# Kernel tuning notes

Measured on AMD Instinct MI355X. Metric: run time of the kernel, lower is better.

The kernel has to match this reference:

```python
import jax, jax.numpy as jnp
import numpy as np

NUM_EMBEDDINGS = 8192
EMBEDDING_DIM = 64
COMMITMENT_COST = 0.25


def setup_inputs() -> dict:
    key = jax.random.key(0)
    kx, ke = jax.random.split(key)
    x = jax.random.normal(kx, (32, 1024, EMBEDDING_DIM), dtype=jnp.float32)
    embeddings = jax.random.normal(ke, (NUM_EMBEDDINGS, EMBEDDING_DIM), dtype=jnp.float32)
    return {"x": x, "embeddings": embeddings}


def reference(x, embeddings):
    d = embeddings.shape[1]
    flat_x = x.reshape(-1, d)  # [N, D]
    # squared euclidean distances (argmin identical to cdist argmin):
    d2 = (
        jnp.sum(flat_x * flat_x, axis=-1, keepdims=True)
        - 2.0 * flat_x @ embeddings.T
        + jnp.sum(embeddings * embeddings, axis=-1)
    )
    encoding_indices = jnp.argmin(d2, axis=1)  # [N]
    quantized = embeddings[encoding_indices].reshape(x.shape)
    codebook_loss = jnp.mean((jax.lax.stop_gradient(quantized) - x) ** 2)
    commitment_loss = COMMITMENT_COST * jnp.mean((quantized - jax.lax.stop_gradient(x)) ** 2)
    loss = codebook_loss + commitment_loss
    # straight-through estimator
    quantized_st = x + jax.lax.stop_gradient(quantized - x)
    return quantized_st, loss, encoding_indices
```

## Files before the change

### kernel.cpp

```cpp
#include <hip/hip_runtime.h>
#include <hip/hip_bf16.h>
#include <float.h>

#define N_ROWS 32768
#define DIMS   64
#define K_EMB  8192
#define NT     (K_EMB / 16)
#define NQ     16
#define NTQ    (NT / NQ)
#define TSTAGE 4
#define NSTAGE (NTQ / TSTAGE)
#define RG     4
#define GAP_THR 1.5e-3f

typedef __attribute__((ext_vector_type(8))) short s8v;
typedef __attribute__((ext_vector_type(4))) float f4v;
typedef __attribute__((ext_vector_type(4))) int   i4v;

#define WS_EFRAG 0
#define WS_EN2   (2 * 1024 * 1024)
#define WS_IDX   (WS_EN2 + K_EMB * 4)
#define WS_KEY   (WS_IDX + N_ROWS * 4)
#define WS_BH    (WS_KEY + N_ROWS * 8)
#define WS_SH    (WS_BH + NQ * N_ROWS * 4)
#define WS_CH    (WS_SH + NQ * N_ROWS * 4)
#define WS_CTL   (WS_CH + NQ * N_ROWS * 4)
#define WS_WL    (WS_CTL + 16)

#define OUT_LOSS (N_ROWS * DIMS)
#define OUT_IDX  (N_ROWS * DIMS + 1)

__device__ inline short bfh(float v) {
    __hip_bfloat16 h = __float2bfloat16(v);
    return __builtin_bit_cast(short, h);
}
__device__ inline float bff(short s) {
    __hip_bfloat16 h = __builtin_bit_cast(__hip_bfloat16, s);
    return __bfloat162float(h);
}

__global__ void vq_prep(const float* __restrict__ emb, short* __restrict__ efrag,
                        float* __restrict__ en2, int4* __restrict__ ctl) {
    if (blockIdx.x == 0 && threadIdx.x == 0) *ctl = make_int4(0, 0, 0, 0);
    int gid = blockIdx.x * 256 + threadIdx.x;
    int t = gid >> 6, lane = gid & 63;
    int m = lane & 15, q = lane >> 4;
    const float* er = emb + (size_t)(t * 16 + m) * DIMS;
    s8v hi0, lo0, hi1, lo1;
    float ss = 0.f;
#pragma unroll
    for (int j = 0; j < 8; ++j) {
        float v0 = er[q * 8 + j];
        float v1 = er[32 + q * 8 + j];
        ss += v0 * v0 + v1 * v1;
        short h0 = bfh(v0); lo0[j] = bfh(v0 - bff(h0)); hi0[j] = h0;
        short h1 = bfh(v1); lo1[j] = bfh(v1 - bff(h1)); hi1[j] = h1;
    }
    s8v* base = (s8v*)efrag + (size_t)t * 4 * 64;
    base[0 * 64 + lane] = hi0;
    base[1 * 64 + lane] = hi1;
    base[2 * 64 + lane] = lo0;
    base[3 * 64 + lane] = lo1;
    ss += __shfl_xor(ss, 16, 64);
    ss += __shfl_xor(ss, 32, 64);
    if (q == 0) en2[t * 16 + m] = -0.5f * ss;
}

__global__ __launch_bounds__(256)
__attribute__((amdgpu_waves_per_eu(2, 3))) void vq_phase1(
    const float* __restrict__ x, const short* __restrict__ efrag,
    const float* __restrict__ en2,
    float* __restrict__ bh, float* __restrict__ sh, int* __restrict__ ch) {
    __shared__ __align__(16) char lds[2][TSTAGE * 4096];
    int tid = threadIdx.x, wid = tid >> 6, lane = tid & 63;
    int m = lane & 15, q = lane >> 4;
    int kh = blockIdx.y;
    int row0 = blockIdx.x * 256 + wid * 64;

    s8v ahi[RG][2], alo[RG][2];
#pragma unroll
    for (int g = 0; g < RG; ++g) {
        const float* xr = x + (size_t)(row0 + g * 16 + m) * DIMS + q * 8;
#pragma unroll
        for (int j = 0; j < 8; ++j) {
            float v0 = xr[j], v1 = xr[32 + j];
            short h0 = bfh(v0); alo[g][0][j] = bfh(v0 - bff(h0)); ahi[g][0][j] = h0;
            short h1 = bfh(v1); alo[g][1][j] = bfh(v1 - bff(h1)); ahi[g][1][j] = h1;
        }
    }

    float best[RG][4], sec[RG][4];
    int bc[RG][4];
#pragma unroll
    for (int g = 0; g < RG; ++g)
#pragma unroll
        for (int r = 0; r < 4; ++r) { best[g][r] = -FLT_MAX; sec[g][r] = -FLT_MAX; bc[g][r] = 0; }

    const char* gsrc = (const char*)efrag + (size_t)kh * NTQ * 4096;

#pragma unroll
    for (int i = 0; i < TSTAGE; ++i)
        __builtin_amdgcn_global_load_lds(
            (const __attribute__((address_space(1))) void*)(gsrc + i * 4096 + tid * 16),
            (__attribute__((address_space(3))) void*)(&lds[0][i * 4096 + tid * 16]),
            16, 0, 0);
    __syncthreads();

    for (int s = 0; s < NSTAGE; ++s) {
        int pb = s & 1;
        if (s + 1 < NSTAGE) {
            const char* gn = gsrc + (size_t)(s + 1) * TSTAGE * 4096;
#pragma unroll
            for (int i = 0; i < TSTAGE; ++i)
                __builtin_amdgcn_global_load_lds(
                    (const __attribute__((address_space(1))) void*)(gn + i * 4096 + tid * 16),
                    (__attribute__((address_space(3))) void*)(&lds[pb ^ 1][i * 4096 + tid * 16]),
                    16, 0, 0);
        }
        const i4v* B = (const i4v*)(lds[pb]);
        int tg0 = kh * NTQ + s * TSTAGE;
        const float* ep = en2 + (size_t)tg0 * 16 + m;
#pragma unroll
        for (int tt = 0; tt < TSTAGE; ++tt) {
            i4v b0 = B[tt * 256 + 0 * 64 + lane];
            i4v b1 = B[tt * 256 + 1 * 64 + lane];
            i4v b2 = B[tt * 256 + 2 * 64 + lane];
            i4v b3 = B[tt * 256 + 3 * 64 + lane];
            float c0 = ep[tt * 16];
            int cidx = (tg0 + tt) * 16 + m;
            f4v cinit = {c0, c0, c0, c0};
#pragma unroll
            for (int g = 0; g < RG; ++g) {
                f4v acc;
                acc = __builtin_amdgcn_mfma_f32_16x16x32_bf16(ahi[g][0], __builtin_bit_cast(s8v, b0), cinit, 0, 0, 0);
                acc = __builtin_amdgcn_mfma_f32_16x16x32_bf16(ahi[g][1], __builtin_bit_cast(s8v, b1), acc, 0, 0, 0);
                acc = __builtin_amdgcn_mfma_f32_16x16x32_bf16(ahi[g][0], __builtin_bit_cast(s8v, b2), acc, 0, 0, 0);
                acc = __builtin_amdgcn_mfma_f32_16x16x32_bf16(ahi[g][1], __builtin_bit_cast(s8v, b3), acc, 0, 0, 0);
                acc = __builtin_amdgcn_mfma_f32_16x16x32_bf16(alo[g][0], __builtin_bit_cast(s8v, b0), acc, 0, 0, 0);
                acc = __builtin_amdgcn_mfma_f32_16x16x32_bf16(alo[g][1], __builtin_bit_cast(s8v, b1), acc, 0, 0, 0);
#pragma unroll
                for (int r = 0; r < 4; ++r) {
                    float v = acc[r];
                    bool gt = v > best[g][r];
                    sec[g][r]  = __builtin_amdgcn_fmed3f(v, sec[g][r], best[g][r]);
                    best[g][r] = fmaxf(best[g][r], v);
                    bc[g][r]   = gt ? cidx : bc[g][r];
                }
            }
        }
        __syncthreads();
    }

#pragma unroll
    for (int g = 0; g < RG; ++g)
#pragma unroll
    for (int r = 0; r < 4; ++r) {
        float b = best[g][r], s = sec[g][r];
        int c = bc[g][r];
#pragma unroll
        for (int off = 1; off < 16; off <<= 1) {
            float ob = __shfl_xor(b, off, 64);
            float os = __shfl_xor(s, off, 64);
            int   oc = __shfl_xor(c, off, 64);
            float nb = fmaxf(b, ob);
            float ns = fmaxf(fminf(b, ob), fmaxf(s, os));
            bool take = (ob > b) || (ob == b && oc < c);
            c = take ? oc : c;
            b = nb; s = ns;
        }
        if (m == 0) {
            int o = kh * N_ROWS + row0 + g * 16 + q * 4 + r;
            bh[o] = b; sh[o] = s; ch[o] = c;
        }
    }
}

__global__ void vq_merge(const float* __restrict__ bh, const float* __restrict__ sh,
                         const int* __restrict__ ch, int* __restrict__ idx_buf,
                         unsigned long long* __restrict__ key8,
                         float* __restrict__ nbv,
                         int* __restrict__ wl, int* __restrict__ wl_count) {
    int row = blockIdx.x * 256 + threadIdx.x;
    float nb = bh[row];
    int   c  = ch[row];
    float ns = -FLT_MAX;
#pragma unroll
    for (int h = 1; h < NQ; ++h) {
        float b = bh[h * N_ROWS + row];
        int   cc = ch[h * N_ROWS + row];
        if (b > nb) { ns = nb; nb = b; c = cc; }
        else        { ns = fmaxf(ns, b); }
    }
#pragma unroll
    for (int h = 0; h < NQ; ++h) ns = fmaxf(ns, sh[h * N_ROWS + row]);
    idx_buf[row] = c;
    key8[row] = 0ULL;
    nbv[row] = nb;
    if (nb - ns < GAP_THR) {
        int pos = atomicAdd(wl_count, 1);
        wl[pos] = row;
    }
}

__global__ __launch_bounds__(64) void vq_fixup(
    const float* __restrict__ x, const float* __restrict__ emb,
    const float* __restrict__ en2, const float* __restrict__ nbv,
    unsigned long long* __restrict__ key8,
    const int* __restrict__ wl, const int* __restrict__ wl_count) {
    int lane = threadIdx.x;
    int cchunk = blockIdx.x & 127;
    int rslice = blockIdx.x >> 7;
    int cnt = *wl_count;
    if (rslice >= cnt) return;
    int c = cchunk * 64 + lane;
    const float4* er = (const float4*)(emb + (size_t)c * DIMS);
    float4 e[16];
#pragma unroll
    for (int qq = 0; qq < 16; ++qq) e[qq] = er[qq];
    float c0 = en2[c];
    for (int wi = rslice; wi < cnt; wi += 16) {
        int row = wl[wi];
        const float4* xr = (const float4*)(x + (size_t)row * DIMS);
        float d = 0.f;
#pragma unroll
        for (int qq = 0; qq < 16; ++qq) {
            float4 ee = e[qq];
            float4 xx = xr[qq];
            d += ee.x * xx.x + ee.y * xx.y + ee.z * xx.z + ee.w * xx.w;
        }
        float bf_ = d + c0;
        int bc_ = c;
#pragma unroll
        for (int off = 1; off < 64; off <<= 1) {
            float of = __shfl_xor(bf_, off, 64);
            int   oc = __shfl_xor(bc_, off, 64);
            if (of > bf_ || (of == bf_ && oc < bc_)) { bf_ = of; bc_ = oc; }
        }
        if (lane == 0 && bf_ >= nbv[row] - GAP_THR) {
            unsigned int u = __float_as_uint(bf_);
            unsigned int sb = ((int)u < 0) ? ~u : (u | 0x80000000u);
            unsigned long long key = ((unsigned long long)sb << 32) | (unsigned int)(~bc_);
            atomicMax(&key8[row], key);
        }
    }
}

__global__ void vq_gather(const float* __restrict__ x, const float* __restrict__ emb,
                          const int* __restrict__ idx_buf,
                          const unsigned long long* __restrict__ key8,
                          float* __restrict__ out, double* __restrict__ loss_acc,
                          int* __restrict__ done_count) {
    int row = blockIdx.x * blockDim.x + threadIdx.x;
    unsigned long long k = key8[row];
    int idx = k ? (int)(~(unsigned int)k) : idx_buf[row];
    const float4* ev = (const float4*)(emb + (size_t)idx * DIMS);
    const float4* xv = (const float4*)(x + (size_t)row * DIMS);
    float4* ov = (float4*)(out + (size_t)row * DIMS);
    float s = 0.f;
#pragma unroll
    for (int qq = 0; qq < 16; ++qq) {
        float4 ee = ev[qq];
        float4 xx = xv[qq];
        float dx = ee.x - xx.x, dy = ee.y - xx.y, dz = ee.z - xx.z, dw = ee.w - xx.w;
        s += dx * dx + dy * dy + dz * dz + dw * dw;
        ov[qq] = ee;
    }
#pragma unroll
    for (int off = 32; off > 0; off >>= 1) s += __shfl_down(s, off, 64);
    if ((threadIdx.x & 63) == 0) atomicAdd(loss_acc, (double)s);
    out[OUT_IDX + row] = (float)idx;
    __syncthreads();
    if (threadIdx.x == 0) {
        __threadfence();
        int d = atomicAdd(done_count, 1);
        if (d == (int)gridDim.x - 1) {
            double total = atomicAdd(loss_acc, 0.0);
            out[OUT_LOSS] = (float)(1.25 * total / (double)(N_ROWS * DIMS));
        }
    }
}

extern "C" void kernel_launch(void* const* d_in, const int* in_sizes, int n_in,
                              void* d_out, int out_size, void* d_ws, size_t ws_size,
                              hipStream_t stream) {
    const float* x   = (const float*)d_in[0];
    const float* emb = (const float*)d_in[1];
    float* out = (float*)d_out;
    char*  ws  = (char*)d_ws;

    short* efrag   = (short*)(ws + WS_EFRAG);
    float* en2     = (float*)(ws + WS_EN2);
    int*   idx_buf = (int*)(ws + WS_IDX);
    unsigned long long* key8 = (unsigned long long*)(ws + WS_KEY);
    float* bhb     = (float*)(ws + WS_BH);
    float* shb     = (float*)(ws + WS_SH);
    int*   chb     = (int*)(ws + WS_CH);
    double* loss_acc = (double*)(ws + WS_CTL);
    int*   wl_count  = (int*)(ws + WS_CTL + 8);
    int*   done_cnt  = (int*)(ws + WS_CTL + 12);
    int*   wl        = (int*)(ws + WS_WL);

    vq_prep<<<(NT * 64) / 256, 256, 0, stream>>>(emb, efrag, en2, (int4*)(ws + WS_CTL));
    vq_phase1<<<dim3(N_ROWS / 256, NQ), 256, 0, stream>>>(x, efrag, en2, bhb, shb, chb);
    vq_merge<<<N_ROWS / 256, 256, 0, stream>>>(bhb, shb, chb, idx_buf, key8, bhb, wl, wl_count);
    vq_fixup<<<2048, 64, 0, stream>>>(x, emb, en2, bhb, key8, wl, wl_count);
    vq_gather<<<N_ROWS / 256, 256, 0, stream>>>(x, emb, idx_buf, key8, out, loss_acc, done_cnt);
}
```

Baseline: 198.1 us.

## Pack tile index into score low bits and halve codebook split count

The tile index within each codebook split is encoded in the low 6 mantissa bits of each distance score. The running argmax then needs only fmax/fmed3 and no separate index register or select, and the cross-lane reduction no longer shuffles indices; the winning lane is found with a ballot. The number of codebook splits drops from 16 to 8 so each split covers 64 tiles, which fits the 6-bit code, and the occupancy hint is widened. The truncated mantissa lowers score precision, so the near-tie threshold for exact re-checking is raised, which may send more rows to the fallback path.

New measurement: 191.3 us. -3.4%, faster.

```diff
diff --git a/kernel.cpp b/kernel.cpp
--- a/kernel.cpp
+++ b/kernel.cpp
@@ -6,12 +6,13 @@
 #define DIMS   64
 #define K_EMB  8192
 #define NT     (K_EMB / 16)
-#define NQ     16
+#define NQ     8
 #define NTQ    (NT / NQ)
 #define TSTAGE 4
 #define NSTAGE (NTQ / TSTAGE)
 #define RG     4
-#define GAP_THR 1.5e-3f
+#define KEYMASK 0xFFFFFFC0u
+#define GAP_THR 3.5e-3f
 
 typedef __attribute__((ext_vector_type(8))) short s8v;
 typedef __attribute__((ext_vector_type(4))) float f4v;
@@ -67,7 +68,7 @@
 }
 
 __global__ __launch_bounds__(256)
-__attribute__((amdgpu_waves_per_eu(2, 3))) void vq_phase1(
+__attribute__((amdgpu_waves_per_eu(2, 4))) void vq_phase1(
     const float* __restrict__ x, const short* __restrict__ efrag,
     const float* __restrict__ en2,
     float* __restrict__ bh, float* __restrict__ sh, int* __restrict__ ch) {
@@ -90,11 +91,10 @@
     }
 
     float best[RG][4], sec[RG][4];
-    int bc[RG][4];
 #pragma unroll
     for (int g = 0; g < RG; ++g)
 #pragma unroll
-        for (int r = 0; r < 4; ++r) { best[g][r] = -FLT_MAX; sec[g][r] = -FLT_MAX; bc[g][r] = 0; }
+        for (int r = 0; r < 4; ++r) { best[g][r] = -FLT_MAX; sec[g][r] = -FLT_MAX; }
 
     const char* gsrc = (const char*)efrag + (size_t)kh * NTQ * 4096;
 
@@ -118,8 +118,7 @@
                     16, 0, 0);
         }
         const i4v* B = (const i4v*)(lds[pb]);
-        int tg0 = kh * NTQ + s * TSTAGE;
-        const float* ep = en2 + (size_t)tg0 * 16 + m;
+        const float* ep = en2 + (size_t)(kh * NTQ + s * TSTAGE) * 16 + m;
 #pragma unroll
         for (int tt = 0; tt < TSTAGE; ++tt) {
             i4v b0 = B[tt * 256 + 0 * 64 + lane];
@@ -127,7 +126,7 @@
             i4v b2 = B[tt * 256 + 2 * 64 + lane];
             i4v b3 = B[tt * 256 + 3 * 64 + lane];
             float c0 = ep[tt * 16];
-            int cidx = (tg0 + tt) * 16 + m;
+            unsigned code = (unsigned)(s * TSTAGE + tt);
             f4v cinit = {c0, c0, c0, c0};
 #pragma unroll
             for (int g = 0; g < RG; ++g) {
@@ -140,11 +139,10 @@
                 acc = __builtin_amdgcn_mfma_f32_16x16x32_bf16(alo[g][1], __builtin_bit_cast(s8v, b1), acc, 0, 0, 0);
 #pragma unroll
                 for (int r = 0; r < 4; ++r) {
-                    float v = acc[r];
-                    bool gt = v > best[g][r];
-                    sec[g][r]  = __builtin_amdgcn_fmed3f(v, sec[g][r], best[g][r]);
-                    best[g][r] = fmaxf(best[g][r], v);
-                    bc[g][r]   = gt ? cidx : bc[g][r];
+                    float kf = __uint_as_float(
+                        (__float_as_uint(acc[r]) & KEYMASK) | code);
+                    sec[g][r]  = __builtin_amdgcn_fmed3f(kf, sec[g][r], best[g][r]);
+                    best[g][r] = fmaxf(best[g][r], kf);
                 }
             }
         }
@@ -155,22 +153,22 @@
     for (int g = 0; g < RG; ++g)
 #pragma unroll
     for (int r = 0; r < 4; ++r) {
-        float b = best[g][r], s = sec[g][r];
-        int c = bc[g][r];
+        float b = best[g][r], sv = sec[g][r];
 #pragma unroll
         for (int off = 1; off < 16; off <<= 1) {
             float ob = __shfl_xor(b, off, 64);
-            float os = __shfl_xor(s, off, 64);
-            int   oc = __shfl_xor(c, off, 64);
-            float nb = fmaxf(b, ob);
-            float ns = fmaxf(fminf(b, ob), fmaxf(s, os));
-            bool take = (ob > b) || (ob == b && oc < c);
-            c = take ? oc : c;
-            b = nb; s = ns;
-        }
-        if (m == 0) {
+            float os = __shfl_xor(sv, off, 64);
+            sv = fmaxf(fminf(b, ob), fmaxf(sv, os));
+            b  = fmaxf(b, ob);
+        }
+        unsigned long long bal =
+            __ballot(__float_as_uint(best[g][r]) == __float_as_uint(b));
+        int win = __ffsll(bal >> (q * 16)) - 1;
+        if (m == win) {
+            int tl  = (int)(__float_as_uint(b) & 63u);
+            int col = ((kh * NTQ + tl) << 4) | m;
             int o = kh * N_ROWS + row0 + g * 16 + q * 4 + r;
-            bh[o] = b; sh[o] = s; ch[o] = c;
+            bh[o] = b; sh[o] = sv; ch[o] = col;
         }
     }
 }
```
